# Kernel optimization log

Measured on AMD Instinct MI355X. Metric: run time of the kernel, lower is better.

The kernel has to match this reference:

```python
import jax, jax.numpy as jnp
import numpy as np
import math

HEAD_DIM = 64
N_Q = 64
N_KV = 8
HIDDEN = 2880
SLIDING = 128
BASE = 150000.0
INIT_CTX = 4096
SCALE = 32.0
NTK_A = 1.0
NTK_B = 32.0
SEQ = 2048


def _rope_cos_sin(position_ids):
    # YaRN-scaled inverse frequencies (scaling_factor > 1 branch)
    freq = BASE ** (jnp.arange(0, HEAD_DIM, 2, dtype=jnp.float32) / HEAD_DIM)
    concentration = 0.1 * math.log(SCALE) + 1.0
    d_half = HEAD_DIM // 2
    low = d_half * math.log(INIT_CTX / (NTK_B * 2 * math.pi)) / math.log(BASE)
    high = d_half * math.log(INIT_CTX / (NTK_A * 2 * math.pi)) / math.log(BASE)
    interpolation = 1.0 / (SCALE * freq)
    extrapolation = 1.0 / freq
    ramp = (jnp.arange(d_half, dtype=jnp.float32) - low) / (high - low)
    mask = 1.0 - jnp.clip(ramp, 0.0, 1.0)
    inv_freq = interpolation * (1.0 - mask) + extrapolation * mask
    freqs = position_ids.astype(jnp.float32)[:, None] * inv_freq[None, :]  # [n, d/2]
    return jnp.cos(freqs) * concentration, jnp.sin(freqs) * concentration


def _apply_rope(x, cos, sin):
    # x: [n, h, d]; cos/sin: [n, d/2]
    cos = cos[:, None, :].astype(x.dtype)
    sin = sin[:, None, :].astype(x.dtype)
    x1, x2 = jnp.split(x, 2, axis=-1)
    return jnp.concatenate([x1 * cos - x2 * sin, x2 * cos + x1 * sin], axis=-1)


def setup_inputs() -> dict:
    key = jax.random.key(0)
    ks = jax.random.split(key, 6)
    qkv_dim = HEAD_DIM * (N_Q + 2 * N_KV)
    return {
        "hidden_states": jax.random.normal(ks[0], (SEQ, HIDDEN), dtype=jnp.float32),
        "qkv_w": jax.random.normal(ks[1], (qkv_dim, HIDDEN), dtype=jnp.float32) * 0.02,
        "qkv_b": jax.random.normal(ks[2], (qkv_dim,), dtype=jnp.float32) * 0.02,
        "o_w": jax.random.normal(ks[3], (HIDDEN, N_Q * HEAD_DIM), dtype=jnp.float32) * 0.02,
        "o_b": jax.random.normal(ks[4], (HIDDEN,), dtype=jnp.float32) * 0.02,
        "sinks": jax.random.normal(ks[5], (N_Q,), dtype=jnp.float32),
        "position_ids": jnp.arange(SEQ, dtype=jnp.int64 if jax.config.jax_enable_x64 else jnp.int32),
    }


def reference(hidden_states, qkv_w, qkv_b, o_w, o_b, sinks, position_ids):
    n = hidden_states.shape[0]
    scaling = HEAD_DIM ** (-0.5)

    # fused QKV projection + split
    qkv = hidden_states @ qkv_w.T + qkv_b  # [n, (nq+2*nkv)*d]
    q_sz, k_sz = N_Q * HEAD_DIM, N_KV * HEAD_DIM
    q = qkv[:, :q_sz].reshape(n, N_Q, HEAD_DIM)
    k = qkv[:, q_sz:q_sz + k_sz].reshape(n, N_KV, HEAD_DIM)
    v = qkv[:, q_sz + k_sz:].reshape(n, N_KV, HEAD_DIM)

    # RoPE (YaRN)
    cos, sin = _rope_cos_sin(position_ids)
    q = _apply_rope(q, cos, sin)
    k = _apply_rope(k, cos, sin)

    # GQA: repeat KV heads to match query heads
    groups = N_Q // N_KV
    k_full = jnp.repeat(k, groups, axis=1)  # [n, N_Q, d]
    v_full = jnp.repeat(v, groups, axis=1)

    scores = jnp.einsum('qhd,khd->hqk', q, k_full) * scaling  # [H, S, S]

    # sliding-window mask (distance > window -> -inf), as in source (no causal term)
    current_pos = position_ids.max()
    key_pos = current_pos - n + 1 + jnp.arange(n)
    dist = position_ids[:, None] - key_pos[None, :]
    win_mask = jnp.where(dist > SLIDING, -jnp.inf, 0.0).astype(scores.dtype)
    scores = scores + win_mask[None, :, :]

    # learned sink logit appended to softmax normalization
    sink = jnp.broadcast_to(sinks[:, None, None], (N_Q, n, 1)).astype(scores.dtype)
    logits = jnp.concatenate([scores, sink], axis=-1)  # [H, S, S+1]
    probs = jax.nn.softmax(logits, axis=-1)[..., :-1]   # drop sink column

    attn = jnp.einsum('hqk,khd->qhd', probs, v_full)    # [S, H, d]
    attn = attn.reshape(n, N_Q * HEAD_DIM)
    return attn @ o_w.T + o_b
```

## Files before the change

### kernel.cpp

```cpp
#include <hip/hip_runtime.h>
#include <hip/hip_bf16.h>
#include <stdint.h>

typedef __attribute__((ext_vector_type(4))) float f32x4;
typedef __attribute__((ext_vector_type(8))) short bf16x8;

#define SEQ 2048
#define HIDDEN 2880
#define NQ 64
#define NKV 8
#define HD 64
#define QKV_DIM 5120
#define Q_SZ 4096
#define K_SZ 512
#define OW_N 2880
#define OW_NPAD 2944
#define OW_K 4096

__device__ __forceinline__ unsigned short f2b_bits(float f) {
    unsigned int x = __float_as_uint(f);
    unsigned int r = (x + 0x7fffu + ((x >> 16) & 1u)) >> 16;
    return (unsigned short)r;
}
__device__ __forceinline__ float b2f(unsigned short u) {
    return __uint_as_float(((unsigned int)u) << 16);
}

__device__ __forceinline__ void llds16(const ushort* g, ushort* l) {
    __builtin_amdgcn_global_load_lds(
        (const __attribute__((address_space(1))) void*)g,
        (__attribute__((address_space(3))) void*)l, 16, 0, 0);
}

__global__ void convert_all(const float* __restrict__ hidden, const float* __restrict__ qkv_w,
                            const float* __restrict__ o_w, ushort* __restrict__ hs_bf,
                            ushort* __restrict__ wqkv_bf, ushort* __restrict__ wo_bf) {
    const int N1 = SEQ * HIDDEN / 4;
    const int N2 = N1 + QKV_DIM * HIDDEN / 4;
    const int N3 = N2 + OW_NPAD * OW_K / 4;
    int i = blockIdx.x * blockDim.x + threadIdx.x;
    int stride = gridDim.x * blockDim.x;
    for (; i < N3; i += stride) {
        const float* src;
        ushort* dst;
        int j;
        if (i < N1) {
            j = i; src = hidden; dst = hs_bf;
        } else if (i < N2) {
            j = i - N1; src = qkv_w; dst = wqkv_bf;
        } else {
            j = i - N2; src = o_w; dst = wo_bf;
            if ((j >> 10) >= OW_N) {
                reinterpret_cast<ushort4*>(dst)[j] = make_ushort4(0, 0, 0, 0);
                continue;
            }
        }
        float4 v = reinterpret_cast<const float4*>(src)[j];
        reinterpret_cast<ushort4*>(dst)[j] =
            make_ushort4(f2b_bits(v.x), f2b_bits(v.y), f2b_bits(v.z), f2b_bits(v.w));
    }
}

template<int OUT_BF16>
__global__ __launch_bounds__(256) void gemm_bt(
    const ushort* __restrict__ A, const ushort* __restrict__ B,
    const float* __restrict__ bias, void* __restrict__ Cout,
    int M, int N, int K, int Nreal, int ldC)
{
    __shared__ __align__(16) ushort As[128 * 64];
    __shared__ __align__(16) ushort Bs[128 * 64];
    const int tid = threadIdx.x;
    const int lane = tid & 63;
    const int w = tid >> 6;
    const int wr = w >> 1, wc = w & 1;

    const int nwg = gridDim.x;
    const int per = nwg >> 3;
    const int wgid = (blockIdx.x & 7) * per + (blockIdx.x >> 3);
    const int m0 = (wgid & 15) * 128;
    const int n0 = (wgid >> 4) * 128;

    f32x4 acc[4][4] = {};

    for (int k0 = 0; k0 < K; k0 += 64) {
        #pragma unroll
        for (int it = 0; it < 4; ++it) {
            int i = it * 256 + tid;
            int row = i >> 3;
            int col16 = (i ^ (row & 7)) & 7;
            const ushort* ga = A + (size_t)(m0 + row) * K + k0 + col16 * 8;
            ushort* la = As + (size_t)(it * 256 + (tid & ~63)) * 8;
            llds16(ga, la);
            const ushort* gb = B + (size_t)(n0 + row) * K + k0 + col16 * 8;
            ushort* lb = Bs + (size_t)(it * 256 + (tid & ~63)) * 8;
            llds16(gb, lb);
        }
        __syncthreads();
        #pragma unroll
        for (int kk = 0; kk < 2; ++kk) {
            bf16x8 a[4], b[4];
            #pragma unroll
            for (int mi = 0; mi < 4; ++mi) {
                int row = wr * 64 + mi * 16 + (lane & 15);
                int byte = row * 128 + kk * 64 + (lane >> 4) * 16;
                byte ^= (row & 7) << 4;
                a[mi] = *reinterpret_cast<const bf16x8*>(reinterpret_cast<const char*>(As) + byte);
            }
            #pragma unroll
            for (int ni = 0; ni < 4; ++ni) {
                int row = wc * 64 + ni * 16 + (lane & 15);
                int byte = row * 128 + kk * 64 + (lane >> 4) * 16;
                byte ^= (row & 7) << 4;
                b[ni] = *reinterpret_cast<const bf16x8*>(reinterpret_cast<const char*>(Bs) + byte);
            }
            #pragma unroll
            for (int mi = 0; mi < 4; ++mi)
                #pragma unroll
                for (int ni = 0; ni < 4; ++ni)
                    acc[mi][ni] = __builtin_amdgcn_mfma_f32_16x16x32_bf16(a[mi], b[ni], acc[mi][ni], 0, 0, 0);
        }
        __syncthreads();
    }

    #pragma unroll
    for (int mi = 0; mi < 4; ++mi) {
        int gr = m0 + wr * 64 + mi * 16 + (lane >> 4) * 4;
        #pragma unroll
        for (int ni = 0; ni < 4; ++ni) {
            int gc = n0 + wc * 64 + ni * 16 + (lane & 15);
            if (gc < Nreal) {
                float bv = bias[gc];
                #pragma unroll
                for (int r = 0; r < 4; ++r) {
                    float v = acc[mi][ni][r] + bv;
                    if (OUT_BF16)
                        ((ushort*)Cout)[(size_t)(gr + r) * ldC + gc] = f2b_bits(v);
                    else
                        ((float*)Cout)[(size_t)(gr + r) * ldC + gc] = v;
                }
            }
        }
    }
}

template<int OUT_BF16>
__global__ __launch_bounds__(256) void gemm_bt64(
    const ushort* __restrict__ A, const ushort* __restrict__ B,
    const float* __restrict__ bias, void* __restrict__ Cout,
    int M, int N, int K, int Nreal, int ldC)
{
    __shared__ __align__(16) ushort As[64 * 64];
    __shared__ __align__(16) ushort Bs[128 * 64];
    const int tid = threadIdx.x;
    const int lane = tid & 63;
    const int w = tid >> 6;
    const int l15 = lane & 15;
    const int l4 = lane >> 4;

    const int nwg = gridDim.x;
    const int per = nwg >> 3;
    const int wgid = (blockIdx.x & 7) * per + (blockIdx.x >> 3);
    const int m0 = (wgid & 31) * 64;
    const int n0 = (wgid >> 5) * 128;

    f32x4 acc[4][2] = {};

    for (int k0 = 0; k0 < K; k0 += 64) {
        #pragma unroll
        for (int it = 0; it < 2; ++it) {
            int i = it * 256 + tid;
            int row = i >> 3;
            int col16 = (i ^ (row & 7)) & 7;
            llds16(A + (size_t)(m0 + row) * K + k0 + col16 * 8,
                   As + (size_t)(it * 256 + (tid & ~63)) * 8);
        }
        #pragma unroll
        for (int it = 0; it < 4; ++it) {
            int i = it * 256 + tid;
            int row = i >> 3;
            int col16 = (i ^ (row & 7)) & 7;
            llds16(B + (size_t)(n0 + row) * K + k0 + col16 * 8,
                   Bs + (size_t)(it * 256 + (tid & ~63)) * 8);
        }
        __syncthreads();
        #pragma unroll
        for (int kk = 0; kk < 2; ++kk) {
            bf16x8 a[4], b[2];
            #pragma unroll
            for (int mi = 0; mi < 4; ++mi) {
                int row = mi * 16 + l15;
                int byte = row * 128 + kk * 64 + l4 * 16;
                byte ^= (row & 7) << 4;
                a[mi] = *reinterpret_cast<const bf16x8*>(reinterpret_cast<const char*>(As) + byte);
            }
            #pragma unroll
            for (int ni = 0; ni < 2; ++ni) {
                int row = w * 32 + ni * 16 + l15;
                int byte = row * 128 + kk * 64 + l4 * 16;
                byte ^= (row & 7) << 4;
                b[ni] = *reinterpret_cast<const bf16x8*>(reinterpret_cast<const char*>(Bs) + byte);
            }
            #pragma unroll
            for (int mi = 0; mi < 4; ++mi)
                #pragma unroll
                for (int ni = 0; ni < 2; ++ni)
                    acc[mi][ni] = __builtin_amdgcn_mfma_f32_16x16x32_bf16(a[mi], b[ni], acc[mi][ni], 0, 0, 0);
        }
        __syncthreads();
    }

    #pragma unroll
    for (int mi = 0; mi < 4; ++mi) {
        int gr = m0 + mi * 16 + l4 * 4;
        #pragma unroll
        for (int ni = 0; ni < 2; ++ni) {
            int gc = n0 + w * 32 + ni * 16 + l15;
            if (gc < Nreal) {
                float bv = bias[gc];
                #pragma unroll
                for (int r = 0; r < 4; ++r) {
                    float v = acc[mi][ni][r] + bv;
                    if (OUT_BF16)
                        ((ushort*)Cout)[(size_t)(gr + r) * ldC + gc] = f2b_bits(v);
                    else
                        ((float*)Cout)[(size_t)(gr + r) * ldC + gc] = v;
                }
            }
        }
    }
}

__global__ __launch_bounds__(256) void rope_kernel(
    const ushort* __restrict__ qkv, const int* __restrict__ pos,
    ushort* __restrict__ q_ro, ushort* __restrict__ k_ro)
{
    __shared__ float cosv[32], sinv[32];
    const int s = blockIdx.x;
    const int tid = threadIdx.x;
    if (tid < 32) {
        int j = tid;
        const float logbase = logf(150000.0f);
        float freq = expf((float)j * (logbase / 32.0f));
        float interp = 1.0f / (32.0f * freq);
        float extrap = 1.0f / freq;
        const float twopi = 6.283185307179586f;
        float low  = 32.0f * logf(4096.0f / (32.0f * twopi)) / logbase;
        float high = 32.0f * logf(4096.0f / (1.0f  * twopi)) / logbase;
        float ramp = ((float)j - low) / (high - low);
        float mask = 1.0f - fminf(fmaxf(ramp, 0.0f), 1.0f);
        float inv_freq = interp * (1.0f - mask) + extrap * mask;
        float ang = (float)pos[s] * inv_freq;
        const float conc = 0.1f * logf(32.0f) + 1.0f;
        cosv[j] = cosf(ang) * conc;
        sinv[j] = sinf(ang) * conc;
    }
    __syncthreads();
    const float qsc = 0.125f * 1.4426950408889634f;
    #pragma unroll
    for (int it = 0; it < 8; ++it) {
        int idx = it * 256 + tid;
        int h = idx >> 5, j = idx & 31;
        const ushort* src = qkv + (size_t)s * QKV_DIM + h * HD;
        float x1 = b2f(src[j]), x2 = b2f(src[j + 32]);
        float c = cosv[j], sn = sinv[j];
        ushort* dst = q_ro + ((size_t)h * SEQ + s) * HD;
        dst[j]      = f2b_bits((x1 * c - x2 * sn) * qsc);
        dst[j + 32] = f2b_bits((x2 * c + x1 * sn) * qsc);
    }
    {
        int h = tid >> 5, j = tid & 31;
        const ushort* src = qkv + (size_t)s * QKV_DIM + Q_SZ + h * HD;
        float x1 = b2f(src[j]), x2 = b2f(src[j + 32]);
        float c = cosv[j], sn = sinv[j];
        ushort* dst = k_ro + ((size_t)h * SEQ + s) * HD;
        dst[j]      = f2b_bits(x1 * c - x2 * sn);
        dst[j + 32] = f2b_bits(x2 * c + x1 * sn);
    }
}

__global__ __launch_bounds__(256) void vtrans_kernel(const ushort* __restrict__ qkv, ushort* __restrict__ vT) {
    __shared__ ushort t[64][65];
    const int kh = blockIdx.x >> 5;
    const int s0 = (blockIdx.x & 31) * 64;
    const int tid = threadIdx.x;
    #pragma unroll
    for (int it = 0; it < 16; ++it) {
        int e = it * 256 + tid;
        int sl = e >> 6, d = e & 63;
        t[d][sl] = qkv[(size_t)(s0 + sl) * QKV_DIM + Q_SZ + K_SZ + kh * HD + d];
    }
    __syncthreads();
    #pragma unroll
    for (int it = 0; it < 16; ++it) {
        int e = it * 256 + tid;
        int d = e >> 6, sl = e & 63;
        vT[((size_t)kh * HD + d) * SEQ + s0 + sl] = t[d][sl];
    }
}

__global__ __launch_bounds__(256, 4) void attn_kernel(
    const ushort* __restrict__ q_ro, const ushort* __restrict__ k_ro,
    const ushort* __restrict__ vT, const float* __restrict__ sinks,
    ushort* __restrict__ attn_out)
{
    __shared__ __align__(16) ushort Kb[2][4096];
    __shared__ __align__(16) ushort Vb[2][4096];
    __shared__ __align__(16) ushort Pl[4][1024];

    const int tid = threadIdx.x;
    const int lane = tid & 63;
    const int w = tid >> 6;
    const int l15 = lane & 15;
    const int l4 = lane >> 4;

    int wg = blockIdx.x;
    int wgid = (wg & 7) * 128 + (wg >> 3);
    const int kh = wgid >> 7;
    const int qh = (wgid >> 4) & 7;
    const int pp = wgid & 15;
    const int h = kh * 8 + qh;

    const float snk = sinks[h];
    char* pbase = (char*)&Pl[w][0];

    const short oneb = (short)0x3F80;
    const bf16x8 bones = {oneb, oneb, oneb, oneb, oneb, oneb, oneb, oneb};

    const int i0 = tid, i1 = 256 + tid;
    const int r0 = i0 >> 3, cs0 = (i0 ^ r0) & 7;
    const int r1 = i1 >> 3, cs1 = (i1 ^ r1) & 7;
    const ushort* gK0 = k_ro + (size_t)kh * (SEQ * 64) + r0 * 64 + cs0 * 8;
    const ushort* gK1 = k_ro + (size_t)kh * (SEQ * 64) + r1 * 64 + cs1 * 8;
    const ushort* gV0 = vT + ((size_t)kh * 64 + r0) * SEQ + cs0 * 8;
    const ushort* gV1 = vT + ((size_t)kh * 64 + r1) * SEQ + cs1 * 8;
    const int ld0 = (tid & ~63) * 8, ld1 = (256 + (tid & ~63)) * 8;

    const int swz = (l15 & 7) << 4;
    const int kvbase = l15 * 128 + ((l4 * 16) ^ swz);
    const int pwbase = l15 * 128 + ((l4 * 8) ^ swz);

    auto stage = [&](int bs, int k0) {
        llds16(gK0 + k0 * 64, &Kb[bs][ld0]);
        llds16(gK1 + k0 * 64, &Kb[bs][ld1]);
        llds16(gV0 + k0,      &Vb[bs][ld0]);
        llds16(gV1 + k0,      &Vb[bs][ld1]);
    };

    for (int sidx = 0; sidx < 2; ++sidx) {
        const int qt = sidx ? (31 - pp) : pp;
        const int q0 = qt * 64;
        const int qw = q0 + w * 16;

        bf16x8 aq[2];
        #pragma unroll
        for (int kc = 0; kc < 2; ++kc)
            aq[kc] = *reinterpret_cast<const bf16x8*>(
                q_ro + ((size_t)h * SEQ + qw + l15) * HD + kc * 32 + l4 * 8);

        f32x4 o[4] = {};
        f32x4 lacc = {0.f, 0.f, 0.f, 0.f};

        const int kt0 = (qt >= 2) ? (qt - 2) : 0;
        int cur = 0;

        stage(0, kt0 * 64);
        __syncthreads();

        for (int kt = kt0; kt < SEQ / 64; ++kt) {
            const int k0 = kt * 64;
            if (kt + 1 < SEQ / 64) stage(cur ^ 1, k0 + 64);

            f32x4 s[4];
            const f32x4 z = {0.f, 0.f, 0.f, 0.f};
            const char* kbp = (const char*)Kb[cur];
            __builtin_amdgcn_s_setprio(1);
            #pragma unroll
            for (int c = 0; c < 4; ++c) {
                bf16x8 bk0 = *reinterpret_cast<const bf16x8*>(kbp + c * 2048 + kvbase);
                s[c] = __builtin_amdgcn_mfma_f32_16x16x32_bf16(bk0, aq[0], z, 0, 0, 0);
                bf16x8 bk1 = *reinterpret_cast<const bf16x8*>(kbp + c * 2048 + (kvbase ^ 64));
                s[c] = __builtin_amdgcn_mfma_f32_16x16x32_bf16(bk1, aq[1], s[c], 0, 0, 0);
            }
            __builtin_amdgcn_s_setprio(0);

            if (k0 < qw - 113) {
                int thr = qw + l15 - 128 - k0;
                #pragma unroll
                for (int c = 0; c < 4; ++c)
                    #pragma unroll
                    for (int r = 0; r < 4; ++r)
                        if (c * 16 + l4 * 4 + r < thr) s[c][r] = -1e30f;
            }

            #pragma unroll
            for (int c = 0; c < 4; ++c) {
                float p0 = exp2f(s[c][0]), p1 = exp2f(s[c][1]);
                float p2 = exp2f(s[c][2]), p3 = exp2f(s[c][3]);
                unsigned int pk0, pk1;
                asm("v_cvt_pk_bf16_f32 %0, %1, %2" : "=v"(pk0) : "v"(p0), "v"(p1));
                asm("v_cvt_pk_bf16_f32 %0, %1, %2" : "=v"(pk1) : "v"(p2), "v"(p3));
                uint2 pv; pv.x = pk0; pv.y = pk1;
                *reinterpret_cast<uint2*>(pbase + (pwbase ^ (c * 32))) = pv;
            }

            const char* vbp = (const char*)Vb[cur];
            __builtin_amdgcn_s_setprio(1);
            #pragma unroll
            for (int kc = 0; kc < 2; ++kc) {
                bf16x8 pa = *reinterpret_cast<const bf16x8*>(pbase + (kvbase ^ (kc * 64)));
                lacc = __builtin_amdgcn_mfma_f32_16x16x32_bf16(pa, bones, lacc, 0, 0, 0);
                #pragma unroll
                for (int df = 0; df < 4; ++df) {
                    bf16x8 bv = *reinterpret_cast<const bf16x8*>(vbp + df * 2048 + (kvbase ^ (kc * 64)));
                    o[df] = __builtin_amdgcn_mfma_f32_16x16x32_bf16(pa, bv, o[df], 0, 0, 0);
                }
            }
            __builtin_amdgcn_s_setprio(0);

            __syncthreads();
            cur ^= 1;
        }

        {
            const float es = exp2f(snk * 1.4426950408889634f);
            float inv[4];
            #pragma unroll
            for (int r = 0; r < 4; ++r) inv[r] = 1.0f / (lacc[r] + es);
            #pragma unroll
            for (int df = 0; df < 4; ++df)
                #pragma unroll
                for (int r = 0; r < 4; ++r) {
                    int row = qw + l4 * 4 + r;
                    int col = df * 16 + l15;
                    attn_out[(size_t)row * Q_SZ + h * HD + col] = f2b_bits(o[df][r] * inv[r]);
                }
        }
    }
}

extern "C" void kernel_launch(void* const* d_in, const int* in_sizes, int n_in,
                              void* d_out, int out_size, void* d_ws, size_t ws_size,
                              hipStream_t stream) {
    const float* hidden = (const float*)d_in[0];
    const float* qkv_w  = (const float*)d_in[1];
    const float* qkv_b  = (const float*)d_in[2];
    const float* o_w    = (const float*)d_in[3];
    const float* o_b    = (const float*)d_in[4];
    const float* sinks  = (const float*)d_in[5];
    const int*   pos    = (const int*)d_in[6];
    float* out = (float*)d_out;

    char* ws = (char*)d_ws;
    size_t off = 0;
    auto alloc = [&](size_t bytes) {
        char* p = ws + off;
        off += (bytes + 255) & ~(size_t)255;
        return p;
    };
    ushort* hs_bf   = (ushort*)alloc((size_t)SEQ * HIDDEN * 2);
    ushort* wqkv_bf = (ushort*)alloc((size_t)QKV_DIM * HIDDEN * 2);
    ushort* qkv_bf  = (ushort*)alloc((size_t)SEQ * QKV_DIM * 2);
    ushort* q_ro    = (ushort*)alloc((size_t)NQ * SEQ * HD * 2);
    ushort* k_ro    = (ushort*)alloc((size_t)NKV * SEQ * HD * 2);
    ushort* vT      = (ushort*)alloc((size_t)NKV * HD * SEQ * 2);
    ushort* attn_bf = (ushort*)alloc((size_t)SEQ * Q_SZ * 2);
    ushort* wo_bf   = (ushort*)alloc((size_t)OW_NPAD * OW_K * 2);

    convert_all<<<2048, 256, 0, stream>>>(hidden, qkv_w, o_w, hs_bf, wqkv_bf, wo_bf);

    gemm_bt<1><<<(QKV_DIM / 128) * (SEQ / 128), 256, 0, stream>>>(
        hs_bf, wqkv_bf, qkv_b, qkv_bf, SEQ, QKV_DIM, HIDDEN, QKV_DIM, QKV_DIM);

    rope_kernel<<<SEQ, 256, 0, stream>>>(qkv_bf, pos, q_ro, k_ro);
    vtrans_kernel<<<NKV * 32, 256, 0, stream>>>(qkv_bf, vT);

    attn_kernel<<<1024, 256, 0, stream>>>(q_ro, k_ro, vT, sinks, attn_bf);

    gemm_bt64<0><<<(OW_NPAD / 128) * (SEQ / 64), 256, 0, stream>>>(
        attn_bf, wo_bf, o_b, out, SEQ, OW_NPAD, OW_K, OW_N, OW_N);
}
```

Before: 255.7 us.

## Fuse RoPE and Q/K head-major scatter into QKV GEMM epilogue

Removes the separate RoPE kernel by applying rotary embedding, bias, and query scaling directly in the QKV GEMM epilogue. Each wave's 64 output columns are one head, so the x1/x2 pairs come from accumulators ni and ni+2. The cos/sin table is precomputed as a tail stage of the conversion kernel. V is written to a compact buffer for the transpose, which avoids writing and rereading the full bf16 QKV intermediate. The cost is scattered 2-byte stores in the epilogue and a per-element cstab load.

```diff
diff --git a/kernel.cpp b/kernel.cpp
--- a/kernel.cpp
+++ b/kernel.cpp
@@ -33,14 +33,34 @@
 }
 
 __global__ void convert_all(const float* __restrict__ hidden, const float* __restrict__ qkv_w,
-                            const float* __restrict__ o_w, ushort* __restrict__ hs_bf,
-                            ushort* __restrict__ wqkv_bf, ushort* __restrict__ wo_bf) {
+                            const float* __restrict__ o_w, const int* __restrict__ pos,
+                            ushort* __restrict__ hs_bf, ushort* __restrict__ wqkv_bf,
+                            ushort* __restrict__ wo_bf, float2* __restrict__ cstab) {
     const int N1 = SEQ * HIDDEN / 4;
     const int N2 = N1 + QKV_DIM * HIDDEN / 4;
     const int N3 = N2 + OW_NPAD * OW_K / 4;
+    const int N4 = N3 + SEQ * 32;
     int i = blockIdx.x * blockDim.x + threadIdx.x;
     int stride = gridDim.x * blockDim.x;
-    for (; i < N3; i += stride) {
+    for (; i < N4; i += stride) {
+        if (i >= N3) {
+            int idx = i - N3;
+            int t = idx >> 5, j = idx & 31;
+            const float logbase = logf(150000.0f);
+            float freq = expf((float)j * (logbase / 32.0f));
+            float interp = 1.0f / (32.0f * freq);
+            float extrap = 1.0f / freq;
+            const float twopi = 6.283185307179586f;
+            float low  = 32.0f * logf(4096.0f / (32.0f * twopi)) / logbase;
+            float high = 32.0f * logf(4096.0f / (1.0f  * twopi)) / logbase;
+            float ramp = ((float)j - low) / (high - low);
+            float mask = 1.0f - fminf(fmaxf(ramp, 0.0f), 1.0f);
+            float inv_freq = interp * (1.0f - mask) + extrap * mask;
+            float ang = (float)pos[t] * inv_freq;
+            const float conc = 0.1f * logf(32.0f) + 1.0f;
+            cstab[idx] = make_float2(cosf(ang) * conc, sinf(ang) * conc);
+            continue;
+        }
         const float* src;
         ushort* dst;
         int j;
@@ -61,11 +81,10 @@
     }
 }
 
-template<int OUT_BF16>
-__global__ __launch_bounds__(256) void gemm_bt(
+__global__ __launch_bounds__(256) void gemm_qkv(
     const ushort* __restrict__ A, const ushort* __restrict__ B,
-    const float* __restrict__ bias, void* __restrict__ Cout,
-    int M, int N, int K, int Nreal, int ldC)
+    const float* __restrict__ bias, const float2* __restrict__ cstab,
+    ushort* __restrict__ q_ro, ushort* __restrict__ k_ro, ushort* __restrict__ v_buf)
 {
     __shared__ __align__(16) ushort As[128 * 64];
     __shared__ __align__(16) ushort Bs[128 * 64];
@@ -73,6 +92,7 @@
     const int lane = tid & 63;
     const int w = tid >> 6;
     const int wr = w >> 1, wc = w & 1;
+    const int K = HIDDEN;
 
     const int nwg = gridDim.x;
     const int per = nwg >> 3;
@@ -88,12 +108,10 @@
             int i = it * 256 + tid;
             int row = i >> 3;
             int col16 = (i ^ (row & 7)) & 7;
-            const ushort* ga = A + (size_t)(m0 + row) * K + k0 + col16 * 8;
-            ushort* la = As + (size_t)(it * 256 + (tid & ~63)) * 8;
-            llds16(ga, la);
-            const ushort* gb = B + (size_t)(n0 + row) * K + k0 + col16 * 8;
-            ushort* lb = Bs + (size_t)(it * 256 + (tid & ~63)) * 8;
-            llds16(gb, lb);
+            llds16(A + (size_t)(m0 + row) * K + k0 + col16 * 8,
+                   As + (size_t)(it * 256 + (tid & ~63)) * 8);
+            llds16(B + (size_t)(n0 + row) * K + k0 + col16 * 8,
+                   Bs + (size_t)(it * 256 + (tid & ~63)) * 8);
         }
         __syncthreads();
         #pragma unroll
@@ -122,22 +140,42 @@
         __syncthreads();
     }
 
+    const int hcol = n0 + wc * 64;
+    const int l15 = lane & 15;
+    const float qsc = 0.125f * 1.4426950408889634f;
     #pragma unroll
     for (int mi = 0; mi < 4; ++mi) {
-        int gr = m0 + wr * 64 + mi * 16 + (lane >> 4) * 4;
-        #pragma unroll
-        for (int ni = 0; ni < 4; ++ni) {
-            int gc = n0 + wc * 64 + ni * 16 + (lane & 15);
-            if (gc < Nreal) {
-                float bv = bias[gc];
+        const int tbase = m0 + wr * 64 + mi * 16 + (lane >> 4) * 4;
+        if (hcol < Q_SZ + K_SZ) {
+            const bool isq = hcol < Q_SZ;
+            const int hh = isq ? (hcol >> 6) : ((hcol - Q_SZ) >> 6);
+            ushort* dst = isq ? (q_ro + (size_t)hh * SEQ * HD)
+                              : (k_ro + (size_t)hh * SEQ * HD);
+            const float scl = isq ? qsc : 1.0f;
+            #pragma unroll
+            for (int ni = 0; ni < 2; ++ni) {
+                const int j = ni * 16 + l15;
+                const float b1 = bias[hcol + j];
+                const float b2 = bias[hcol + j + 32];
                 #pragma unroll
                 for (int r = 0; r < 4; ++r) {
-                    float v = acc[mi][ni][r] + bv;
-                    if (OUT_BF16)
-                        ((ushort*)Cout)[(size_t)(gr + r) * ldC + gc] = f2b_bits(v);
-                    else
-                        ((float*)Cout)[(size_t)(gr + r) * ldC + gc] = v;
+                    const int t = tbase + r;
+                    float2 cs = cstab[t * 32 + j];
+                    float x1 = acc[mi][ni][r] + b1;
+                    float x2 = acc[mi][ni + 2][r] + b2;
+                    dst[(size_t)t * HD + j]      = f2b_bits((x1 * cs.x - x2 * cs.y) * scl);
+                    dst[(size_t)t * HD + j + 32] = f2b_bits((x2 * cs.x + x1 * cs.y) * scl);
                 }
+            }
+        } else {
+            const int vb = hcol - (Q_SZ + K_SZ);
+            #pragma unroll
+            for (int ni = 0; ni < 4; ++ni) {
+                const int col = vb + ni * 16 + l15;
+                const float bv = bias[hcol + ni * 16 + l15];
+                #pragma unroll
+                for (int r = 0; r < 4; ++r)
+                    v_buf[(size_t)(tbase + r) * K_SZ + col] = f2b_bits(acc[mi][ni][r] + bv);
             }
         }
     }
@@ -230,55 +268,7 @@
     }
 }
 
-__global__ __launch_bounds__(256) void rope_kernel(
-    const ushort* __restrict__ qkv, const int* __restrict__ pos,
-    ushort* __restrict__ q_ro, ushort* __restrict__ k_ro)
-{
-    __shared__ float cosv[32], sinv[32];
-    const int s = blockIdx.x;
-    const int tid = threadIdx.x;
-    if (tid < 32) {
-        int j = tid;
-        const float logbase = logf(150000.0f);
-        float freq = expf((float)j * (logbase / 32.0f));
-        float interp = 1.0f / (32.0f * freq);
-        float extrap = 1.0f / freq;
-        const float twopi = 6.283185307179586f;
-        float low  = 32.0f * logf(4096.0f / (32.0f * twopi)) / logbase;
-        float high = 32.0f * logf(4096.0f / (1.0f  * twopi)) / logbase;
-        float ramp = ((float)j - low) / (high - low);
-        float mask = 1.0f - fminf(fmaxf(ramp, 0.0f), 1.0f);
-        float inv_freq = interp * (1.0f - mask) + extrap * mask;
-        float ang = (float)pos[s] * inv_freq;
-        const float conc = 0.1f * logf(32.0f) + 1.0f;
-        cosv[j] = cosf(ang) * conc;
-        sinv[j] = sinf(ang) * conc;
-    }
-    __syncthreads();
-    const float qsc = 0.125f * 1.4426950408889634f;
-    #pragma unroll
-    for (int it = 0; it < 8; ++it) {
-        int idx = it * 256 + tid;
-        int h = idx >> 5, j = idx & 31;
-        const ushort* src = qkv + (size_t)s * QKV_DIM + h * HD;
-        float x1 = b2f(src[j]), x2 = b2f(src[j + 32]);
-        float c = cosv[j], sn = sinv[j];
-        ushort* dst = q_ro + ((size_t)h * SEQ + s) * HD;
-        dst[j]      = f2b_bits((x1 * c - x2 * sn) * qsc);
-        dst[j + 32] = f2b_bits((x2 * c + x1 * sn) * qsc);
-    }
-    {
-        int h = tid >> 5, j = tid & 31;
-        const ushort* src = qkv + (size_t)s * QKV_DIM + Q_SZ + h * HD;
-        float x1 = b2f(src[j]), x2 = b2f(src[j + 32]);
-        float c = cosv[j], sn = sinv[j];
-        ushort* dst = k_ro + ((size_t)h * SEQ + s) * HD;
-        dst[j]      = f2b_bits(x1 * c - x2 * sn);
-        dst[j + 32] = f2b_bits(x2 * c + x1 * sn);
-    }
-}
-
-__global__ __launch_bounds__(256) void vtrans_kernel(const ushort* __restrict__ qkv, ushort* __restrict__ vT) {
+__global__ __launch_bounds__(256) void vtrans_kernel(const ushort* __restrict__ v_buf, ushort* __restrict__ vT) {
     __shared__ ushort t[64][65];
     const int kh = blockIdx.x >> 5;
     const int s0 = (blockIdx.x & 31) * 64;
@@ -287,7 +277,7 @@
     for (int it = 0; it < 16; ++it) {
         int e = it * 256 + tid;
         int sl = e >> 6, d = e & 63;
-        t[d][sl] = qkv[(size_t)(s0 + sl) * QKV_DIM + Q_SZ + K_SZ + kh * HD + d];
+        t[d][sl] = v_buf[(size_t)(s0 + sl) * K_SZ + kh * HD + d];
     }
     __syncthreads();
     #pragma unroll
@@ -459,20 +449,20 @@
     };
     ushort* hs_bf   = (ushort*)alloc((size_t)SEQ * HIDDEN * 2);
     ushort* wqkv_bf = (ushort*)alloc((size_t)QKV_DIM * HIDDEN * 2);
-    ushort* qkv_bf  = (ushort*)alloc((size_t)SEQ * QKV_DIM * 2);
+    float2* cstab   = (float2*)alloc((size_t)SEQ * 32 * sizeof(float2));
+    ushort* v_buf   = (ushort*)alloc((size_t)SEQ * K_SZ * 2);
     ushort* q_ro    = (ushort*)alloc((size_t)NQ * SEQ * HD * 2);
     ushort* k_ro    = (ushort*)alloc((size_t)NKV * SEQ * HD * 2);
     ushort* vT      = (ushort*)alloc((size_t)NKV * HD * SEQ * 2);
     ushort* attn_bf = (ushort*)alloc((size_t)SEQ * Q_SZ * 2);
     ushort* wo_bf   = (ushort*)alloc((size_t)OW_NPAD * OW_K * 2);
 
-    convert_all<<<2048, 256, 0, stream>>>(hidden, qkv_w, o_w, hs_bf, wqkv_bf, wo_bf);
-
-    gemm_bt<1><<<(QKV_DIM / 128) * (SEQ / 128), 256, 0, stream>>>(
-        hs_bf, wqkv_bf, qkv_b, qkv_bf, SEQ, QKV_DIM, HIDDEN, QKV_DIM, QKV_DIM);
-
-    rope_kernel<<<SEQ, 256, 0, stream>>>(qkv_bf, pos, q_ro, k_ro);
-    vtrans_kernel<<<NKV * 32, 256, 0, stream>>>(qkv_bf, vT);
+    convert_all<<<2048, 256, 0, stream>>>(hidden, qkv_w, o_w, pos, hs_bf, wqkv_bf, wo_bf, cstab);
+
+    gemm_qkv<<<(QKV_DIM / 128) * (SEQ / 128), 256, 0, stream>>>(
+        hs_bf, wqkv_bf, qkv_b, cstab, q_ro, k_ro, v_buf);
+
+    vtrans_kernel<<<NKV * 32, 256, 0, stream>>>(v_buf, vT);
 
     attn_kernel<<<1024, 256, 0, stream>>>(q_ro, k_ro, vT, sinks, attn_bf);
 
```

Result: slower. 276.0 us (+7.9%).
